# Performance work log

Hardware: AMD Instinct MI355X
Metric: run time of the kernel (lower is better)

The kernel has to match this reference:

```python
import jax, jax.numpy as jnp
import numpy as np

T, D, F, E, K = 2048, 512, 2048, 8, 2


def setup_inputs() -> dict:
    key = jax.random.key(0)
    ks = jax.random.split(key, 5)
    scaled = lambda k, shape, fan: jax.random.normal(k, shape, jnp.float32) * (fan ** -0.5)
    x = jax.random.normal(ks[0], (T, D), jnp.float32)
    Wg = scaled(ks[1], (D, E), D)          # gate: Linear(D -> E), no bias
    W1 = scaled(ks[2], (E, D, F), D)       # per-expert up proj
    W3 = scaled(ks[3], (E, D, F), D)       # per-expert gate proj (SwiGLU)
    W2 = scaled(ks[4], (E, F, D), F)       # per-expert down proj
    return {"x": x, "Wg": Wg, "W1": W1, "W2": W2, "W3": W3}


def reference(x, Wg, W1, W2, W3):
    # gate logits + top-k routing (topk over raw logits, softmax over the k picked logits,
    # computed in float32 then cast back -- matches the torch source)
    logits = x @ Wg                                   # [T, E]
    topw, sel = jax.lax.top_k(logits, K)              # [T, K] each
    weights = jax.nn.softmax(topw.astype(jnp.float32), axis=-1).astype(x.dtype)
    out = jnp.zeros_like(x)
    # NOTE: the source uses `output[batch_idx] = ...` (assignment, not +=), so later
    # experts OVERWRITE earlier ones for tokens routed to multiple experts.
    # We replicate that exactly with sequential jnp.where overwrites.
    for i in range(E):
        hit = sel == i                                # [T, K]
        mask = hit.any(axis=-1)                       # [T] tokens routed to expert i
        w_i = jnp.sum(jnp.where(hit, weights, 0.0), axis=-1)  # [T] routing weight
        h = jax.nn.silu(x @ W1[i]) * (x @ W3[i])      # [T, F] SwiGLU
        y = h @ W2[i]                                 # [T, D]
        out = jnp.where(mask[:, None], w_i[:, None] * y, out)
    return out
```

## Files before the change

### kernel.cpp

```cpp
#include <hip/hip_runtime.h>
#include <hip/hip_bf16.h>
#include <math.h>

typedef __attribute__((ext_vector_type(8))) short short8;
typedef __attribute__((ext_vector_type(4))) float f32x4;

#define T_TOK 2048
#define D_DIM 512
#define F_DIM 2048
#define E_NUM 8
#define MAXT1 40

__device__ __forceinline__ unsigned short f2bf(float f) {
  union { float f; unsigned u; } c; c.f = f;
  unsigned u = c.u;
  return (unsigned short)((u + 0x7fffu + ((u >> 16) & 1u)) >> 16);
}

__device__ __forceinline__ void gld16(const void* g, void* l) {
  __builtin_amdgcn_global_load_lds((const __attribute__((address_space(1))) int*)g,
                                   (__attribute__((address_space(3))) int*)l, 16, 0, 0);
}

__global__ __launch_bounds__(256) void k_prep(const float* __restrict__ xin,
                                              const float* __restrict__ Wg,
                                              const float* __restrict__ W1,
                                              const float* __restrict__ W3,
                                              int* __restrict__ jbuf,
                                              float* __restrict__ wbuf,
                                              unsigned short* __restrict__ xb,
                                              unsigned short* __restrict__ w1f,
                                              unsigned short* __restrict__ w3f) {
  __shared__ float4 tile4[2][64 * 32];
  int bz = blockIdx.x, tid = threadIdx.x;

  if (bz < 256) {
    int gid = bz * 256 + tid;
    int t = gid >> 5, seg = gid & 31;
    const float* xp = xin + (size_t)t * D_DIM + seg * 16;
    unsigned short* xo = xb + (size_t)t * D_DIM + seg * 16;
    float acc[8];
#pragma unroll
    for (int e = 0; e < 8; ++e) acc[e] = 0.f;
#pragma unroll
    for (int i = 0; i < 4; ++i) {
      float4 v = *(const float4*)(xp + i * 4);
      ushort4 o;
      o.x = f2bf(v.x); o.y = f2bf(v.y); o.z = f2bf(v.z); o.w = f2bf(v.w);
      *(ushort4*)(xo + i * 4) = o;
      const float* xs = (const float*)&v;
#pragma unroll
      for (int q = 0; q < 4; ++q) {
        int d = seg * 16 + i * 4 + q;
        const float4* wr = (const float4*)(Wg + (size_t)d * 8);
        float4 w0 = wr[0], w1 = wr[1];
        acc[0] += xs[q] * w0.x; acc[1] += xs[q] * w0.y;
        acc[2] += xs[q] * w0.z; acc[3] += xs[q] * w0.w;
        acc[4] += xs[q] * w1.x; acc[5] += xs[q] * w1.y;
        acc[6] += xs[q] * w1.z; acc[7] += xs[q] * w1.w;
      }
    }
#pragma unroll
    for (int off = 1; off < 32; off <<= 1)
#pragma unroll
      for (int e = 0; e < 8; ++e) acc[e] += __shfl_xor(acc[e], off);
    if (seg == 0) {
      float l0 = -1e30f, l1 = -1e30f; int i0 = 0, i1 = 0;
#pragma unroll
      for (int e = 0; e < 8; ++e) {
        float l = acc[e];
        if (l > l0) { l1 = l0; i1 = i0; l0 = l; i0 = e; }
        else if (l > l1) { l1 = l; i1 = e; }
      }
      int j; float w;
      if (i0 > i1) { j = i0; w = 1.f / (1.f + expf(l1 - l0)); }
      else         { j = i1; w = 1.f / (1.f + expf(l0 - l1)); }
      jbuf[t] = j; wbuf[t] = w;
    }
    return;
  }

  int idx = bz - 256;
  int z = idx >> 6, rem = idx & 63;
  const int K = 512, N = 2048;
  int n0 = (rem & 15) * 128, k0 = (rem >> 4) * 128;
  size_t zsz = (size_t)(K / 32) * (N / 16) * 512;
  const float* in; unsigned short* out;
  if (z < 8) { in = W1 + (size_t)z * K * N;       out = w1f + (size_t)z * zsz; }
  else       { in = W3 + (size_t)(z - 8) * K * N; out = w3f + (size_t)(z - 8) * zsz; }

  int lr = tid >> 5, lc = tid & 31;
  int wv = tid >> 6, l = tid & 63;
  int n4l = (l & 15) >> 2, nr = l & 3, kg = (l >> 4) * 8;

  auto loadT = [&](int buf, int kb0) {
#pragma unroll
    for (int it = 0; it < 8; ++it) {
      int row = it * 8 + lr;
      float4 v = *(const float4*)(in + (size_t)(kb0 + row) * N + n0 + lc * 4);
      tile4[buf][row * 32 + ((lc + (row >> 3) * 4) & 31)] = v;
    }
  };
  auto storeT = [&](int buf, int kb0) {
    const float* tf = (const float*)&tile4[buf][0];
#pragma unroll
    for (int q = 0; q < 4; ++q) {
      int fid = wv * 4 + q;
      int nb = fid >> 1, kb = fid & 1;
      int n4 = nb * 4 + n4l;
      short8 o;
#pragma unroll
      for (int j = 0; j < 8; ++j) {
        int k = kb * 32 + kg + j;
        int slot = k * 32 + ((n4 + (k >> 3) * 4) & 31);
        o[j] = (short)f2bf(tf[slot * 4 + nr]);
      }
      unsigned short* op = out + (((size_t)(n0 / 16 + nb) * (K / 32)) + (kb0 / 32 + kb)) * 512 + l * 8;
      *(short8*)op = o;
    }
  };

  loadT(0, k0);
  __syncthreads();
  loadT(1, k0 + 64);
  storeT(0, k0);
  __syncthreads();
  storeT(1, k0 + 64);
}

__global__ __launch_bounds__(256) void k_bucket(const int* __restrict__ jbuf,
                                                int* __restrict__ cntp,
                                                int* __restrict__ basep,
                                                int* __restrict__ list,
                                                int* __restrict__ tl1,
                                                int* __restrict__ ntl) {
  __shared__ int scnt[8], scur[8];
  int tid = threadIdx.x;
  if (tid < 8) scnt[tid] = 0;
  __syncthreads();
  for (int t = tid; t < T_TOK; t += 256) atomicAdd(&scnt[jbuf[t]], 1);
  __syncthreads();
  if (tid == 0) {
    int run = 0;
    for (int e = 0; e < 8; ++e) {
      cntp[e] = scnt[e]; basep[e] = run; scur[e] = run;
      run += scnt[e];
    }
    int n1 = 0, bb = 0;
    for (int e = 0; e < 8; ++e) {
      for (int m = 0; m < scnt[e]; m += 64) tl1[n1++] = (e << 16) | (bb + m);
      bb += scnt[e];
    }
    ntl[0] = n1;
  }
  __syncthreads();
  for (int t = tid; t < T_TOK; t += 256) {
    int j = jbuf[t];
    int p = atomicAdd(&scur[j], 1);
    list[p] = t;
  }
}

__global__ __launch_bounds__(256, 2) void k_ffn1w2(const unsigned short* __restrict__ xb,
                                                   const unsigned short* __restrict__ w1f,
                                                   const unsigned short* __restrict__ w3f,
                                                   const float* __restrict__ W2,
                                                   unsigned short* __restrict__ w2f,
                                                   const int* __restrict__ cntp,
                                                   const int* __restrict__ basep,
                                                   const int* __restrict__ list,
                                                   const int* __restrict__ tl1,
                                                   const int* __restrict__ ntl,
                                                   unsigned short* __restrict__ hbuf) {
  __shared__ __align__(16) unsigned short sA[64 * 512];
  int tid = threadIdx.x, wv = tid >> 6, l = tid & 63;

  if (blockIdx.x >= 1280) {
    int idx = blockIdx.x - 1280;
    int z = idx >> 6, rem = idx & 63;
    const int K = 2048, N = 512;
    int n0 = (rem & 3) * 128, k0 = (rem >> 2) * 128;
    size_t zsz = (size_t)(K / 32) * (N / 16) * 512;
    const float* in = W2 + (size_t)z * K * N;
    unsigned short* out = w2f + (size_t)z * zsz;
    float4* tile4 = (float4*)sA;

    int lr = tid >> 5, lc = tid & 31;
    int n4l = (l & 15) >> 2, nr = l & 3, kg = (l >> 4) * 8;

    auto loadT = [&](int buf, int kb0) {
#pragma unroll
      for (int it = 0; it < 8; ++it) {
        int row = it * 8 + lr;
        float4 v = *(const float4*)(in + (size_t)(kb0 + row) * N + n0 + lc * 4);
        tile4[buf * 2048 + row * 32 + ((lc + (row >> 3) * 4) & 31)] = v;
      }
    };
    auto storeT = [&](int buf, int kb0) {
      const float* tf = (const float*)&tile4[buf * 2048];
#pragma unroll
      for (int q = 0; q < 4; ++q) {
        int fid = wv * 4 + q;
        int nb = fid >> 1, kb = fid & 1;
        int n4 = nb * 4 + n4l;
        short8 o;
#pragma unroll
        for (int j = 0; j < 8; ++j) {
          int k = kb * 32 + kg + j;
          int slot = k * 32 + ((n4 + (k >> 3) * 4) & 31);
          o[j] = (short)f2bf(tf[slot * 4 + nr]);
        }
        unsigned short* op = out + (((size_t)(n0 / 16 + nb) * (K / 32)) + (kb0 / 32 + kb)) * 512 + l * 8;
        *(short8*)op = o;
      }
    };

    loadT(0, k0);
    __syncthreads();
    loadT(1, k0 + 64);
    storeT(0, k0);
    __syncthreads();
    storeT(1, k0 + 64);
    return;
  }

  int L = blockIdx.x;
  int b = (L & 7) * 160 + (L >> 3);
  int x = b % 40, y = b / 40;
  if (x >= ntl[0]) return;
  int pk = tl1[x];
  int e = pk >> 16, g0 = pk & 0xffff;
  int lim = basep[e] + cntp[e];

#pragma unroll
  for (int it = 0; it < 16; ++it) {
    int row = wv * 16 + it;
    int gr = g0 + row; if (gr >= lim) gr = lim - 1;
    int tok = list[gr];
    int slot = (l & 56) | ((l & 7) ^ (row & 7));
    gld16(xb + (size_t)tok * D_DIM + slot * 8, sA + row * 512);
  }

  const unsigned short* w1b = w1f + ((size_t)(e * 128 + y * 4 + wv) * 16) * 512 + l * 8;
  const unsigned short* w3b = w3f + ((size_t)(e * 128 + y * 4 + wv) * 16) * 512 + l * 8;

  short8 P1[4], P3[4], Q1[4], Q3[4], R1[4], R3[4];
  auto loadS = [&](short8* r1, short8* r3, int s) {
#pragma unroll
    for (int q = 0; q < 4; ++q) {
      r1[q] = *(const short8*)(w1b + (size_t)(s * 4 + q) * 512);
      r3[q] = *(const short8*)(w3b + (size_t)(s * 4 + q) * 512);
    }
  };

  f32x4 au[4], av[4];
#pragma unroll
  for (int i = 0; i < 4; ++i) {
    au[i] = (f32x4){0.f, 0.f, 0.f, 0.f};
    av[i] = (f32x4){0.f, 0.f, 0.f, 0.f};
  }

  auto quartC = [&](const short8* r1, const short8* r3, int s) {
#pragma unroll
    for (int q = 0; q < 4; ++q) {
      int kf = s * 4 + q;
      short8 a[4];
#pragma unroll
      for (int i = 0; i < 4; ++i) {
        int r = i * 16 + (l & 15);
        int slot = kf * 4 + (l >> 4);
        int swz = (slot & 56) | ((slot & 7) ^ (r & 7));
        a[i] = *(const short8*)(sA + r * 512 + swz * 8);
      }
#pragma unroll
      for (int i = 0; i < 4; ++i) {
        au[i] = __builtin_amdgcn_mfma_f32_16x16x32_bf16(a[i], r1[q], au[i], 0, 0, 0);
        av[i] = __builtin_amdgcn_mfma_f32_16x16x32_bf16(a[i], r3[q], av[i], 0, 0, 0);
      }
    }
  };

  loadS(P1, P3, 0);
  loadS(Q1, Q3, 1);
  __syncthreads();
  loadS(R1, R3, 2);
  quartC(P1, P3, 0);
  loadS(P1, P3, 3);
  quartC(Q1, Q3, 1);
  quartC(R1, R3, 2);
  quartC(P1, P3, 3);

  int cloc = l & 15, rb = (l >> 4) * 4;
  int col = y * 64 + wv * 16 + cloc;
#pragma unroll
  for (int i = 0; i < 4; ++i)
#pragma unroll
    for (int r = 0; r < 4; ++r) {
      int gr = g0 + i * 16 + rb + r;
      if (gr < lim) {
        float uu = au[i][r], vv = av[i][r];
        float hh = (uu / (1.f + expf(-uu))) * vv;
        hbuf[(size_t)gr * F_DIM + col] = f2bf(hh);
      }
    }
}

__global__ __launch_bounds__(256, 3) void k_ffn2(const unsigned short* __restrict__ hbuf,
                                                 const unsigned short* __restrict__ w2f,
                                                 const int* __restrict__ cntp,
                                                 const int* __restrict__ basep,
                                                 const int* __restrict__ list,
                                                 const int* __restrict__ tl1,
                                                 const int* __restrict__ ntl,
                                                 const float* __restrict__ wbuf,
                                                 float* __restrict__ out) {
  int L = blockIdx.x;
  int c = L & 7, q = L >> 3;
  int x = c * 5 + (q % 5);
  int nt = q / 5;
  if (x >= ntl[0]) return;
  int pk = tl1[x];
  int e = pk >> 16, g0 = pk & 0xffff;
  int lim = basep[e] + cntp[e];
  __shared__ unsigned short sA[2 * 8192];
  int tid = threadIdx.x, wv = tid >> 6, l = tid & 63;
  int wr = wv >> 1, wc = wv & 1;

  auto stage = [&](int buf, int ck) {
#pragma unroll
    for (int it = 0; it < 4; ++it) {
      int row0 = it * 16 + wv * 4;
      int row = row0 + (l >> 4);
      int gr = g0 + row; if (gr > T_TOK - 1) gr = T_TOK - 1;
      int sl = (l & 8) | ((l & 7) ^ (row & 7));
      gld16(hbuf + (size_t)gr * F_DIM + ck * 128 + sl * 8, sA + buf * 8192 + row0 * 128);
    }
  };

  const unsigned short* b2p = w2f + ((size_t)(e * 32 + nt * 2 + wc) * 64) * 512 + l * 8;

  short8 Ba[4], Bb[4];
  auto loadB = [&](short8* B, int ck) {
#pragma unroll
    for (int kk = 0; kk < 4; ++kk)
      B[kk] = *(const short8*)(b2p + (size_t)(ck * 4 + kk) * 512);
  };

  f32x4 acc[2];
  acc[0] = (f32x4){0.f, 0.f, 0.f, 0.f};
  acc[1] = (f32x4){0.f, 0.f, 0.f, 0.f};

  auto compute = [&](const short8* B, int cur) {
#pragma unroll
    for (int kk = 0; kk < 4; ++kk) {
      short8 a[2];
#pragma unroll
      for (int i = 0; i < 2; ++i) {
        int r = wr * 32 + i * 16 + (l & 15);
        int slot = kk * 4 + (l >> 4);
        int swz = (slot & 8) | ((slot & 7) ^ (r & 7));
        a[i] = *(const short8*)(sA + cur * 8192 + r * 128 + swz * 8);
      }
      acc[0] = __builtin_amdgcn_mfma_f32_16x16x32_bf16(a[0], B[kk], acc[0], 0, 0, 0);
      acc[1] = __builtin_amdgcn_mfma_f32_16x16x32_bf16(a[1], B[kk], acc[1], 0, 0, 0);
    }
  };

  stage(0, 0);
  loadB(Ba, 0);
  __syncthreads();
  int cur = 0;
  for (int ck = 0; ck < 16; ck += 2) {
    stage(cur ^ 1, ck + 1);
    loadB(Bb, ck + 1);
    compute(Ba, cur);
    __syncthreads();
    cur ^= 1;
    if (ck + 2 < 16) {
      stage(cur ^ 1, ck + 2);
      loadB(Ba, ck + 2);
    }
    compute(Bb, cur);
    __syncthreads();
    cur ^= 1;
  }

  int cloc = l & 15, rb = (l >> 4) * 4;
#pragma unroll
  for (int i = 0; i < 2; ++i)
#pragma unroll
    for (int r = 0; r < 4; ++r) {
      int gr = g0 + wr * 32 + i * 16 + rb + r;
      if (gr < lim) {
        int tok = list[gr];
        out[(size_t)tok * D_DIM + nt * 32 + wc * 16 + cloc] = wbuf[tok] * acc[i][r];
      }
    }
}

extern "C" void kernel_launch(void* const* d_in, const int* in_sizes, int n_in,
                              void* d_out, int out_size, void* d_ws, size_t ws_size,
                              hipStream_t stream) {
  const float* x  = (const float*)d_in[0];
  const float* Wg = (const float*)d_in[1];
  const float* W1 = (const float*)d_in[2];
  const float* W2 = (const float*)d_in[3];
  const float* W3 = (const float*)d_in[4];
  float* out = (float*)d_out;
  char* ws = (char*)d_ws;

  int*            jbuf  = (int*)(ws + 0);
  float*          wbuf  = (float*)(ws + 8192);
  int*            cntp  = (int*)(ws + 16384);
  int*            basep = (int*)(ws + 16448);
  int*            list  = (int*)(ws + 16640);
  int*            tl1   = (int*)(ws + 24832);
  int*            ntl   = (int*)(ws + 25600);
  unsigned short* xb    = (unsigned short*)(ws + 32768);
  unsigned short* w1f   = (unsigned short*)(ws + 32768 + 2097152);
  unsigned short* w3f   = (unsigned short*)(ws + 32768 + 2097152 + 16777216);
  unsigned short* w2f   = (unsigned short*)(ws + 32768 + 2097152 + 2 * 16777216);
  unsigned short* hbuf  = (unsigned short*)(ws + 32768 + 2097152 + 3 * 16777216);

  k_prep<<<dim3(1280), dim3(256), 0, stream>>>(x, Wg, W1, W3, jbuf, wbuf, xb, w1f, w3f);
  k_bucket<<<dim3(1), dim3(256), 0, stream>>>(jbuf, cntp, basep, list, tl1, ntl);
  k_ffn1w2<<<dim3(1792), dim3(256), 0, stream>>>(xb, w1f, w3f, W2, w2f, cntp, basep, list, tl1, ntl, hbuf);
  k_ffn2<<<dim3(640), dim3(256), 0, stream>>>(hbuf, w2f, cntp, basep, list, tl1, ntl, wbuf, out);
}
```

Baseline: 75.00 us.

## Halve FFN1 token tile to 32 rows and split W2 conversion blocks

```diff
diff --git a/kernel.cpp b/kernel.cpp
--- a/kernel.cpp
+++ b/kernel.cpp
@@ -10,6 +10,7 @@
 #define F_DIM 2048
 #define E_NUM 8
 #define MAXT1 40
+#define MAXT32 80
 
 __device__ __forceinline__ unsigned short f2bf(float f) {
   union { float f; unsigned u; } c; c.f = f;
@@ -133,6 +134,7 @@
                                                 int* __restrict__ basep,
                                                 int* __restrict__ list,
                                                 int* __restrict__ tl1,
+                                                int* __restrict__ tl32,
                                                 int* __restrict__ ntl) {
   __shared__ int scnt[8], scur[8];
   int tid = threadIdx.x;
@@ -152,6 +154,12 @@
       bb += scnt[e];
     }
     ntl[0] = n1;
+    int n2 = 0; bb = 0;
+    for (int e = 0; e < 8; ++e) {
+      for (int m = 0; m < scnt[e]; m += 32) tl32[n2++] = (e << 16) | (bb + m);
+      bb += scnt[e];
+    }
+    ntl[1] = n2;
   }
   __syncthreads();
   for (int t = tid; t < T_TOK; t += 256) {
@@ -161,7 +169,7 @@
   }
 }
 
-__global__ __launch_bounds__(256, 2) void k_ffn1w2(const unsigned short* __restrict__ xb,
+__global__ __launch_bounds__(256, 4) void k_ffn1w2(const unsigned short* __restrict__ xb,
                                                    const unsigned short* __restrict__ w1f,
                                                    const unsigned short* __restrict__ w3f,
                                                    const float* __restrict__ W2,
@@ -169,17 +177,17 @@
                                                    const int* __restrict__ cntp,
                                                    const int* __restrict__ basep,
                                                    const int* __restrict__ list,
-                                                   const int* __restrict__ tl1,
+                                                   const int* __restrict__ tl32,
                                                    const int* __restrict__ ntl,
                                                    unsigned short* __restrict__ hbuf) {
-  __shared__ __align__(16) unsigned short sA[64 * 512];
+  __shared__ __align__(16) unsigned short sA[32 * 512];
   int tid = threadIdx.x, wv = tid >> 6, l = tid & 63;
 
-  if (blockIdx.x >= 1280) {
-    int idx = blockIdx.x - 1280;
-    int z = idx >> 6, rem = idx & 63;
+  if (blockIdx.x >= 2560) {
+    int idx = blockIdx.x - 2560;
+    int z = idx >> 7, rem = idx & 127;
     const int K = 2048, N = 512;
-    int n0 = (rem & 3) * 128, k0 = (rem >> 2) * 128;
+    int n0 = (rem & 3) * 128, k0 = (rem >> 2) * 64;
     size_t zsz = (size_t)(K / 32) * (N / 16) * 512;
     const float* in = W2 + (size_t)z * K * N;
     unsigned short* out = w2f + (size_t)z * zsz;
@@ -187,54 +195,43 @@
 
     int lr = tid >> 5, lc = tid & 31;
     int n4l = (l & 15) >> 2, nr = l & 3, kg = (l >> 4) * 8;
-
-    auto loadT = [&](int buf, int kb0) {
-#pragma unroll
-      for (int it = 0; it < 8; ++it) {
-        int row = it * 8 + lr;
-        float4 v = *(const float4*)(in + (size_t)(kb0 + row) * N + n0 + lc * 4);
-        tile4[buf * 2048 + row * 32 + ((lc + (row >> 3) * 4) & 31)] = v;
-      }
-    };
-    auto storeT = [&](int buf, int kb0) {
-      const float* tf = (const float*)&tile4[buf * 2048];
-#pragma unroll
-      for (int q = 0; q < 4; ++q) {
-        int fid = wv * 4 + q;
-        int nb = fid >> 1, kb = fid & 1;
-        int n4 = nb * 4 + n4l;
-        short8 o;
-#pragma unroll
-        for (int j = 0; j < 8; ++j) {
-          int k = kb * 32 + kg + j;
-          int slot = k * 32 + ((n4 + (k >> 3) * 4) & 31);
-          o[j] = (short)f2bf(tf[slot * 4 + nr]);
-        }
-        unsigned short* op = out + (((size_t)(n0 / 16 + nb) * (K / 32)) + (kb0 / 32 + kb)) * 512 + l * 8;
-        *(short8*)op = o;
-      }
-    };
-
-    loadT(0, k0);
+#pragma unroll
+    for (int it = 0; it < 8; ++it) {
+      int row = it * 8 + lr;
+      float4 v = *(const float4*)(in + (size_t)(k0 + row) * N + n0 + lc * 4);
+      tile4[row * 32 + ((lc + (row >> 3) * 4) & 31)] = v;
+    }
     __syncthreads();
-    loadT(1, k0 + 64);
-    storeT(0, k0);
-    __syncthreads();
-    storeT(1, k0 + 64);
+    const float* tf = (const float*)tile4;
+#pragma unroll
+    for (int q = 0; q < 4; ++q) {
+      int fid = wv * 4 + q;
+      int nb = fid >> 1, kb = fid & 1;
+      int n4 = nb * 4 + n4l;
+      short8 o;
+#pragma unroll
+      for (int j = 0; j < 8; ++j) {
+        int k = kb * 32 + kg + j;
+        int slot = k * 32 + ((n4 + (k >> 3) * 4) & 31);
+        o[j] = (short)f2bf(tf[slot * 4 + nr]);
+      }
+      unsigned short* op = out + (((size_t)(n0 / 16 + nb) * (K / 32)) + (k0 / 32 + kb)) * 512 + l * 8;
+      *(short8*)op = o;
+    }
     return;
   }
 
   int L = blockIdx.x;
-  int b = (L & 7) * 160 + (L >> 3);
-  int x = b % 40, y = b / 40;
-  if (x >= ntl[0]) return;
-  int pk = tl1[x];
+  int b = (L & 7) * 320 + (L >> 3);
+  int x = b % 80, y = b / 80;
+  if (x >= ntl[1]) return;
+  int pk = tl32[x];
   int e = pk >> 16, g0 = pk & 0xffff;
   int lim = basep[e] + cntp[e];
 
 #pragma unroll
-  for (int it = 0; it < 16; ++it) {
-    int row = wv * 16 + it;
+  for (int it = 0; it < 8; ++it) {
+    int row = wv * 8 + it;
     int gr = g0 + row; if (gr >= lim) gr = lim - 1;
     int tok = list[gr];
     int slot = (l & 56) | ((l & 7) ^ (row & 7));
@@ -244,7 +241,7 @@
   const unsigned short* w1b = w1f + ((size_t)(e * 128 + y * 4 + wv) * 16) * 512 + l * 8;
   const unsigned short* w3b = w3f + ((size_t)(e * 128 + y * 4 + wv) * 16) * 512 + l * 8;
 
-  short8 P1[4], P3[4], Q1[4], Q3[4], R1[4], R3[4];
+  short8 P1[4], P3[4], Q1[4], Q3[4];
   auto loadS = [&](short8* r1, short8* r3, int s) {
 #pragma unroll
     for (int q = 0; q < 4; ++q) {
@@ -253,9 +250,9 @@
     }
   };
 
-  f32x4 au[4], av[4];
-#pragma unroll
-  for (int i = 0; i < 4; ++i) {
+  f32x4 au[2], av[2];
+#pragma unroll
+  for (int i = 0; i < 2; ++i) {
     au[i] = (f32x4){0.f, 0.f, 0.f, 0.f};
     av[i] = (f32x4){0.f, 0.f, 0.f, 0.f};
   }
@@ -264,16 +261,16 @@
 #pragma unroll
     for (int q = 0; q < 4; ++q) {
       int kf = s * 4 + q;
-      short8 a[4];
-#pragma unroll
-      for (int i = 0; i < 4; ++i) {
+      short8 a[2];
+#pragma unroll
+      for (int i = 0; i < 2; ++i) {
         int r = i * 16 + (l & 15);
         int slot = kf * 4 + (l >> 4);
         int swz = (slot & 56) | ((slot & 7) ^ (r & 7));
         a[i] = *(const short8*)(sA + r * 512 + swz * 8);
       }
 #pragma unroll
-      for (int i = 0; i < 4; ++i) {
+      for (int i = 0; i < 2; ++i) {
         au[i] = __builtin_amdgcn_mfma_f32_16x16x32_bf16(a[i], r1[q], au[i], 0, 0, 0);
         av[i] = __builtin_amdgcn_mfma_f32_16x16x32_bf16(a[i], r3[q], av[i], 0, 0, 0);
       }
@@ -281,19 +278,19 @@
   };
 
   loadS(P1, P3, 0);
+  __syncthreads();
   loadS(Q1, Q3, 1);
-  __syncthreads();
-  loadS(R1, R3, 2);
   quartC(P1, P3, 0);
-  loadS(P1, P3, 3);
+  loadS(P1, P3, 2);
   quartC(Q1, Q3, 1);
-  quartC(R1, R3, 2);
-  quartC(P1, P3, 3);
+  loadS(Q1, Q3, 3);
+  quartC(P1, P3, 2);
+  quartC(Q1, Q3, 3);
 
   int cloc = l & 15, rb = (l >> 4) * 4;
   int col = y * 64 + wv * 16 + cloc;
 #pragma unroll
-  for (int i = 0; i < 4; ++i)
+  for (int i = 0; i < 2; ++i)
 #pragma unroll
     for (int r = 0; r < 4; ++r) {
       int gr = g0 + i * 16 + rb + r;
@@ -415,6 +412,7 @@
   int*            basep = (int*)(ws + 16448);
   int*            list  = (int*)(ws + 16640);
   int*            tl1   = (int*)(ws + 24832);
+  int*            tl32  = (int*)(ws + 25088);
   int*            ntl   = (int*)(ws + 25600);
   unsigned short* xb    = (unsigned short*)(ws + 32768);
   unsigned short* w1f   = (unsigned short*)(ws + 32768 + 2097152);
@@ -423,7 +421,7 @@
   unsigned short* hbuf  = (unsigned short*)(ws + 32768 + 2097152 + 3 * 16777216);
 
   k_prep<<<dim3(1280), dim3(256), 0, stream>>>(x, Wg, W1, W3, jbuf, wbuf, xb, w1f, w3f);
-  k_bucket<<<dim3(1), dim3(256), 0, stream>>>(jbuf, cntp, basep, list, tl1, ntl);
-  k_ffn1w2<<<dim3(1792), dim3(256), 0, stream>>>(xb, w1f, w3f, W2, w2f, cntp, basep, list, tl1, ntl, hbuf);
+  k_bucket<<<dim3(1), dim3(256), 0, stream>>>(jbuf, cntp, basep, list, tl1, tl32, ntl);
+  k_ffn1w2<<<dim3(3584), dim3(256), 0, stream>>>(xb, w1f, w3f, W2, w2f, cntp, basep, list, tl32, ntl, hbuf);
   k_ffn2<<<dim3(640), dim3(256), 0, stream>>>(hbuf, w2f, cntp, basep, list, tl1, ntl, wbuf, out);
 }
```

Measured after the change: 75.94 us. No clear change (+1.3%).
